# Kernel optimization log

Measured on AMD Instinct MI355X. Metric: run time of the kernel, lower is better.

The kernel has to match this reference:

```python
import jax, jax.numpy as jnp
import numpy as np

B, T, H, D = 1, 2048, 32, 64
SCALE = 0.015625  # 1/64 = 1/head_size
DEG = 2


def setup_inputs() -> dict:
    key = jax.random.key(0)
    k1, k2, k3, k4 = jax.random.split(key, 4)
    q = jax.random.normal(k1, (B, T, H, D), dtype=jnp.float32)
    k = jax.random.normal(k2, (B, T, H, D), dtype=jnp.float32)
    v = jax.random.normal(k3, (B, T, H, D), dtype=jnp.float32)
    # log_G: per-token, per-head log decay (must be <= 0)
    g = -0.1 * jax.random.uniform(k4, (B, T, H), dtype=jnp.float32)
    return {"q": q, "k": k, "v": v, "g": g}


def reference(q, k, v, g):
    # q,k,v: [B,T,H,D]; g: [B,T,H] log-decay (log_G)
    # Power retention, deg=2, attention (quadratic) form for T <= switch_over_seq_len.
    g_cum = jnp.cumsum(g, axis=1)                         # [B,T,H]
    gc = jnp.transpose(g_cum, (0, 2, 1))                  # [B,H,T]
    # decay weight exp(gc[t]-gc[s]) for s<=t, 0 otherwise
    log_decay = gc[:, :, :, None] - gc[:, :, None, :]     # [B,H,T,S]
    causal = jnp.tril(jnp.ones((T, T), dtype=bool))
    decay = jnp.where(causal, jnp.exp(log_decay), 0.0)    # [B,H,T,S]
    qk = jnp.einsum("bthd,bshd->bhts", q, k) * SCALE      # [B,H,T,S]
    w = (qk ** DEG) * decay                               # nonneg scores, deg=2
    num = jnp.einsum("bhts,bshd->bthd", w, v)             # [B,T,H,D]
    denom = jnp.transpose(w.sum(-1), (0, 2, 1))           # [B,T,H]
    out = num / jnp.maximum(denom, 1.0)[..., None]
    return out
```

## Files before the change

kernel.cpp:

```cpp
#include <hip/hip_runtime.h>

#define T_DIM 2048
#define H_DIM 32
#define D_DIM 64
#define SCALE_F 0.015625f
#define TILE_STRIDE 2048

typedef unsigned short ushort;
typedef __attribute__((ext_vector_type(8))) short short8;
typedef __attribute__((ext_vector_type(16))) float f32x16;
typedef __attribute__((ext_vector_type(2))) float f32x2;
typedef __attribute__((ext_vector_type(4))) float f32x4;

#define MFMA32(A, B, C) __builtin_amdgcn_mfma_f32_32x32x16_bf16((A), (B), (C), 0, 0, 0)

__global__ __launch_bounds__(256)
void cumsum_g_kernel(const float* __restrict__ g, float* __restrict__ gc) {
    const int h = blockIdx.x;
    const int tid = threadIdx.x;
    const int PER = T_DIM / 256;

    __shared__ float sums[256];

    float loc[8];
    float run = 0.f;
    const int t0 = tid * PER;
    for (int i = 0; i < PER; ++i) {
        run += g[(size_t)(t0 + i) * H_DIM + h];
        loc[i] = run;
    }
    sums[tid] = run;
    __syncthreads();

    for (int off = 1; off < 256; off <<= 1) {
        float vv = (tid >= off) ? sums[tid - off] : 0.f;
        __syncthreads();
        sums[tid] += vv;
        __syncthreads();
    }
    float excl = (tid == 0) ? 0.f : sums[tid - 1];

    for (int i = 0; i < PER; ++i)
        gc[(size_t)h * T_DIM + t0 + i] = excl + loc[i];
}

__device__ __forceinline__ ushort f2bf(float x) {
    unsigned u = __float_as_uint(x);
    unsigned r = (u + 0x7fffu + ((u >> 16) & 1u)) >> 16;
    return (ushort)r;
}

__global__ __launch_bounds__(256)
void prep_kernel(const float* __restrict__ q, const float* __restrict__ k,
                 const float* __restrict__ v, const float* __restrict__ gc,
                 ushort* __restrict__ qfrag, ushort* __restrict__ kfrag,
                 ushort* __restrict__ vfrag) {
    __shared__ ushort qt_l[64 * 64];
    __shared__ ushort kt_l[64 * 64];

    const int h   = blockIdx.x;
    const int tt  = blockIdx.y;
    const int tid = threadIdx.x;

    {
        const int r    = tid >> 2;
        const int dseg = (tid & 3) * 16;
        const int t    = tt * 64 + r;
        const float gct = gc[(size_t)h * T_DIM + t];
        const float eq = SCALE_F * __expf(0.5f * gct);
        const float ek = __expf(-0.5f * gct);
        const float* qp = q + ((size_t)t * H_DIM + h) * 64 + dseg;
        const float* kp = k + ((size_t)t * H_DIM + h) * 64 + dseg;
        union { ushort u[16]; uint4 uu[2]; } oq, ok;
#pragma unroll
        for (int i = 0; i < 16; ++i) {
            oq.u[i] = f2bf(qp[i] * eq);
            ok.u[i] = f2bf(kp[i] * ek);
        }
        const int c0 = (tid & 3) * 2;
#pragma unroll
        for (int cc = 0; cc < 2; ++cc) {
            const int slot = (c0 + cc) ^ (r & 7);
            *reinterpret_cast<uint4*>(&qt_l[r * 64 + slot * 8]) = oq.uu[cc];
            *reinterpret_cast<uint4*>(&kt_l[r * 64 + slot * 8]) = ok.uu[cc];
        }
    }
    __syncthreads();

#pragma unroll
    for (int n = 0; n < 2; ++n) {
        const int ch   = tid + 256 * n;
        const int l31  = ch & 31;
        const int hi   = (ch >> 5) & 1;
        const int ks   = (ch >> 6) & 3;
        const int t32r = ch >> 8;
        const int row  = t32r * 32 + l31;
        const int slot = (2 * ks + hi) ^ (row & 7);
        uint4 qq = *reinterpret_cast<const uint4*>(&qt_l[row * 64 + slot * 8]);
        uint4 kk = *reinterpret_cast<const uint4*>(&kt_l[row * 64 + slot * 8]);
        const size_t base = ((size_t)h * 64 + tt * 2 + t32r) * TILE_STRIDE
                          + (size_t)(((ks * 2 + hi) * 32) + l31) * 8;
        *reinterpret_cast<uint4*>(qfrag + base) = qq;
        *reinterpret_cast<uint4*>(kfrag + base) = kk;
    }

#pragma unroll
    for (int n = 0; n < 2; ++n) {
        const int c9   = (tid >> 5) + 8 * n;
        const int l31  = tid & 31;
        const int hi   = c9 & 1;
        const int kh2  = (c9 >> 1) & 1;
        const int dblk = (c9 >> 2) & 1;
        const int s32r = c9 >> 3;
        const int tb = tt * 64 + s32r * 32 + kh2 * 16 + hi * 8;
        union { ushort u[8]; uint4 uu; } ov;
#pragma unroll
        for (int j = 0; j < 8; ++j)
            ov.u[j] = f2bf(v[((size_t)(tb + j) * H_DIM + h) * 64 + dblk * 32 + l31]);
        const size_t base = ((size_t)h * 64 + tt * 2 + s32r) * TILE_STRIDE
                          + (size_t)((((dblk * 2 + kh2) * 2 + hi) * 32) + l31) * 8;
        *reinterpret_cast<uint4*>(vfrag + base) = ov.uu;
    }
}

__device__ __forceinline__ short8 ld8(const ushort* p) {
    return *reinterpret_cast<const short8*>(p);
}

__device__ __forceinline__ unsigned cvt_pk_bf16(float lo, float hi) {
    unsigned r;
    asm("v_cvt_pk_bf16_f32 %0, %1, %2" : "=v"(r) : "v"(lo), "v"(hi));
    return r;
}

__device__ __forceinline__ short8 pack_w2(const f32x2* w2) {
    unsigned p0 = cvt_pk_bf16(w2[0][0], w2[0][1]);
    unsigned p1 = cvt_pk_bf16(w2[1][0], w2[1][1]);
    unsigned p2 = cvt_pk_bf16(w2[2][0], w2[2][1]);
    unsigned p3 = cvt_pk_bf16(w2[3][0], w2[3][1]);
    asm("v_permlane32_swap_b32 %0, %1" : "+v"(p0), "+v"(p2));
    asm("v_permlane32_swap_b32 %0, %1" : "+v"(p1), "+v"(p3));
    union { unsigned u[4]; short8 s; } af;
    af.u[0] = p0; af.u[1] = p1; af.u[2] = p2; af.u[3] = p3;
    return af.s;
}

__device__ __forceinline__ void gll16(const void* g, void* l) {
    __builtin_amdgcn_global_load_lds(
        (const __attribute__((address_space(1))) unsigned int*)g,
        (__attribute__((address_space(3))) unsigned int*)l, 16, 0, 0);
}

__device__ __forceinline__ void stage32k(ushort* dst, const char* ksrc,
                                         const char* vsrc, int tid) {
    char* d = (char*)dst + (tid >> 6) * 1024;
    const int lo = tid * 16;
    gll16(ksrc + lo,        d);
    gll16(ksrc + 8192 + lo, d + 8192);
    gll16(vsrc + lo,        d + 16384);
    gll16(vsrc + 8192 + lo, d + 24576);
}

template<int MODE>
__device__ __forceinline__ void unit32(
    const ushort* ldsK, const ushort* ldsV,
    int lofs, int hi, int l31,
    const short8 (&qr)[4], f32x16& o0, f32x16& o1, f32x2& den2)
{
    const short8 kf0 = ld8(ldsK + lofs);
    const short8 kf1 = ld8(ldsK + 512 + lofs);
    const short8 kf2 = ld8(ldsK + 1024 + lofs);
    const short8 kf3 = ld8(ldsK + 1536 + lofs);
    const short8 vf0 = ld8(ldsV + lofs);
    const short8 vf1 = ld8(ldsV + 512 + lofs);
    const short8 vf2 = ld8(ldsV + 1024 + lofs);
    const short8 vf3 = ld8(ldsV + 1536 + lofs);

    f32x16 c;
#pragma unroll
    for (int i = 0; i < 16; ++i) c[i] = 0.f;
    c = MFMA32(kf0, qr[0], c);
    c = MFMA32(kf1, qr[1], c);
    c = MFMA32(kf2, qr[2], c);
    c = MFMA32(kf3, qr[3], c);

    f32x2 w2[8];
#pragma unroll
    for (int i = 0; i < 8; ++i) {
        const int r0 = 2 * i;
        f32x2 x; x[0] = c[r0]; x[1] = c[r0 + 1];
        f32x2 ww = x * x;
        if (MODE == 1) {
            const int sl0 = (r0 & 3) + 8 * (r0 >> 2) + 4 * hi;
            ww[0] = (sl0 <= l31) ? ww[0] : 0.f;
            ww[1] = (sl0 + 1 <= l31) ? ww[1] : 0.f;
        }
        w2[i] = ww;
        den2 += ww;
    }
    const short8 a0 = pack_w2(&w2[0]);
    o0 = MFMA32(a0, vf0, o0);
    o1 = MFMA32(a0, vf2, o1);
    const short8 a1 = pack_w2(&w2[4]);
    o0 = MFMA32(a1, vf1, o0);
    o1 = MFMA32(a1, vf3, o1);
}

__global__ __launch_bounds__(512, 4)
void retention_mfma_kernel(const ushort* __restrict__ qfrag,
                           const ushort* __restrict__ kfrag,
                           const ushort* __restrict__ vfrag,
                           float* __restrict__ out) {
    __shared__ ushort buf[2][16384];

    const int bid = blockIdx.x;
    const int h   = (bid & 7) + 8 * ((bid >> 3) & 3);
    const int r   = bid >> 5;
    const int qb  = (r < 8) ? (2 * r) : (31 - 2 * r + 16 - 16);
    const int qbb = (r < 8) ? (2 * r) : (31 - 2 * (r - 8) - 16 + 16);
    (void)qb; (void)qbb;
    const int QB  = (r < 8) ? (2 * r) : (15 - 2 * (r - 8));

    const int tid = threadIdx.x;
    const int w   = tid >> 6;
    const int qi  = w & 3;
    const int si  = w >> 2;
    const int lane = tid & 63;
    const int hi  = lane >> 5;
    const int l31 = lane & 31;
    const int lofs = hi * 256 + l31 * 8;
    const int myT32 = 4 * QB + qi;

    short8 qr[4];
    {
        const ushort* qp = qfrag + ((size_t)h * 64 + myT32) * TILE_STRIDE;
#pragma unroll
        for (int ks = 0; ks < 4; ++ks) qr[ks] = ld8(qp + ks * 512 + lofs);
    }

    f32x16 o0, o1;
#pragma unroll
    for (int i = 0; i < 16; ++i) { o0[i] = 0.f; o1[i] = 0.f; }
    f32x2 d2; d2[0] = 0.f; d2[1] = 0.f;

    const char* kgb = (const char*)(kfrag + (size_t)h * 64 * TILE_STRIDE);
    const char* vgb = (const char*)(vfrag + (size_t)h * 64 * TILE_STRIDE);

    stage32k(buf[0], kgb, vgb, tid);
    __syncthreads();

    for (int J = 0; J <= QB; ++J) {
        if (J < QB)
            stage32k(buf[(J + 1) & 1], kgb + (size_t)(J + 1) * 16384,
                     vgb + (size_t)(J + 1) * 16384, tid);

        const ushort* bK = buf[J & 1];
        const ushort* bV = bK + 8192;
        const int c1 = 4 * J + si;
        const int c2 = c1 + 2;

        if (c1 < myT32)
            unit32<0>(bK + si * 2048, bV + si * 2048, lofs, hi, l31, qr, o0, o1, d2);
        else if (c1 == myT32)
            unit32<1>(bK + si * 2048, bV + si * 2048, lofs, hi, l31, qr, o0, o1, d2);

        if (c2 < myT32)
            unit32<0>(bK + (2 + si) * 2048, bV + (2 + si) * 2048, lofs, hi, l31, qr, o0, o1, d2);
        else if (c2 == myT32)
            unit32<1>(bK + (2 + si) * 2048, bV + (2 + si) * 2048, lofs, hi, l31, qr, o0, o1, d2);

        __syncthreads();
    }

    float* pm  = (float*)(&buf[0][0]);
    float* pmd = (float*)(&buf[1][0]);

    float den = d2[0] + d2[1];
    den += __shfl_xor(den, 32);
    if (hi == 0) pmd[(qi * 2 + si) * 32 + l31] = den;

    if (si == 0) {
#pragma unroll
        for (int rr = 0; rr < 16; ++rr) {
            const int row = (rr & 3) + 8 * (rr >> 2) + 4 * hi;
            pm[(qi * 32 + row) * 64 + l31]      = o0[rr];
            pm[(qi * 32 + row) * 64 + 32 + l31] = o1[rr];
        }
    }
    __syncthreads();
    if (si == 1) {
#pragma unroll
        for (int rr = 0; rr < 16; ++rr) {
            const int row = (rr & 3) + 8 * (rr >> 2) + 4 * hi;
            pm[(qi * 32 + row) * 64 + l31]      += o0[rr];
            pm[(qi * 32 + row) * 64 + 32 + l31] += o1[rr];
        }
    }
    __syncthreads();

    {
        const int row  = tid >> 2;
        const int qq   = row >> 5;
        const int r32  = row & 31;
        const int dseg = (tid & 3) * 16;
        const float dtot = pmd[(qq * 2 + 0) * 32 + r32] + pmd[(qq * 2 + 1) * 32 + r32];
        const float inv = 1.f / fmaxf(dtot, 1.f);
        const float* src = pm + (qq * 32 + r32) * 64 + dseg;
        float* dst = out + ((size_t)(QB * 128 + row) * H_DIM + h) * 64 + dseg;
#pragma unroll
        for (int jv = 0; jv < 4; ++jv) {
            f32x4 s = *reinterpret_cast<const f32x4*>(src + 4 * jv);
            s *= inv;
            *reinterpret_cast<f32x4*>(dst + 4 * jv) = s;
        }
    }
}

extern "C" void kernel_launch(void* const* d_in, const int* in_sizes, int n_in,
                              void* d_out, int out_size, void* d_ws, size_t ws_size,
                              hipStream_t stream) {
    const float* q = (const float*)d_in[0];
    const float* k = (const float*)d_in[1];
    const float* v = (const float*)d_in[2];
    const float* g = (const float*)d_in[3];
    float* out = (float*)d_out;

    const size_t GC_BYTES = (size_t)H_DIM * T_DIM * sizeof(float);
    const size_t BF_ELEMS = (size_t)H_DIM * T_DIM * D_DIM;

    float* gc = (float*)d_ws;
    ushort* qfrag = (ushort*)((char*)d_ws + GC_BYTES);
    ushort* kfrag = qfrag + BF_ELEMS;
    ushort* vfrag = kfrag + BF_ELEMS;

    cumsum_g_kernel<<<H_DIM, 256, 0, stream>>>(g, gc);
    prep_kernel<<<dim3(H_DIM, T_DIM / 64), 256, 0, stream>>>(q, k, v, gc,
                                                             qfrag, kfrag, vfrag);
    retention_mfma_kernel<<<512, 512, 0, stream>>>(qfrag, kfrag, vfrag, out);
}
```

Baseline: 46.56 us.

## Fuse bf16 prep into retention kernel with register-staged fp32 K/V loads

Removes the separate prep kernel that converted q/k/v to bf16 fragment layout in workspace. The main kernel now loads fp32 Q, K and V directly, applies the decay scaling and converts to bf16 in registers, and writes into a smaller double-buffered LDS tile of 64 keys per step. Global loads for the next tile are issued before compute and written to LDS after it, replacing the async global_load_lds staging. It also reorders block scheduling so the largest query blocks launch first. This saves a launch and a global round trip of the bf16 intermediates. In exchange each block re-reads fp32 K/V (twice the bytes), redoes the conversion, and runs twice as many barrier-synchronised iterations.

```diff
diff --git a/kernel.cpp b/kernel.cpp
--- a/kernel.cpp
+++ b/kernel.cpp
@@ -4,7 +4,7 @@
 #define H_DIM 32
 #define D_DIM 64
 #define SCALE_F 0.015625f
-#define TILE_STRIDE 2048
+#define ROWSTRIDE 2048
 
 typedef unsigned short ushort;
 typedef __attribute__((ext_vector_type(8))) short short8;
@@ -42,85 +42,6 @@
 
     for (int i = 0; i < PER; ++i)
         gc[(size_t)h * T_DIM + t0 + i] = excl + loc[i];
-}
-
-__device__ __forceinline__ ushort f2bf(float x) {
-    unsigned u = __float_as_uint(x);
-    unsigned r = (u + 0x7fffu + ((u >> 16) & 1u)) >> 16;
-    return (ushort)r;
-}
-
-__global__ __launch_bounds__(256)
-void prep_kernel(const float* __restrict__ q, const float* __restrict__ k,
-                 const float* __restrict__ v, const float* __restrict__ gc,
-                 ushort* __restrict__ qfrag, ushort* __restrict__ kfrag,
-                 ushort* __restrict__ vfrag) {
-    __shared__ ushort qt_l[64 * 64];
-    __shared__ ushort kt_l[64 * 64];
-
-    const int h   = blockIdx.x;
-    const int tt  = blockIdx.y;
-    const int tid = threadIdx.x;
-
-    {
-        const int r    = tid >> 2;
-        const int dseg = (tid & 3) * 16;
-        const int t    = tt * 64 + r;
-        const float gct = gc[(size_t)h * T_DIM + t];
-        const float eq = SCALE_F * __expf(0.5f * gct);
-        const float ek = __expf(-0.5f * gct);
-        const float* qp = q + ((size_t)t * H_DIM + h) * 64 + dseg;
-        const float* kp = k + ((size_t)t * H_DIM + h) * 64 + dseg;
-        union { ushort u[16]; uint4 uu[2]; } oq, ok;
-#pragma unroll
-        for (int i = 0; i < 16; ++i) {
-            oq.u[i] = f2bf(qp[i] * eq);
-            ok.u[i] = f2bf(kp[i] * ek);
-        }
-        const int c0 = (tid & 3) * 2;
-#pragma unroll
-        for (int cc = 0; cc < 2; ++cc) {
-            const int slot = (c0 + cc) ^ (r & 7);
-            *reinterpret_cast<uint4*>(&qt_l[r * 64 + slot * 8]) = oq.uu[cc];
-            *reinterpret_cast<uint4*>(&kt_l[r * 64 + slot * 8]) = ok.uu[cc];
-        }
-    }
-    __syncthreads();
-
-#pragma unroll
-    for (int n = 0; n < 2; ++n) {
-        const int ch   = tid + 256 * n;
-        const int l31  = ch & 31;
-        const int hi   = (ch >> 5) & 1;
-        const int ks   = (ch >> 6) & 3;
-        const int t32r = ch >> 8;
-        const int row  = t32r * 32 + l31;
-        const int slot = (2 * ks + hi) ^ (row & 7);
-        uint4 qq = *reinterpret_cast<const uint4*>(&qt_l[row * 64 + slot * 8]);
-        uint4 kk = *reinterpret_cast<const uint4*>(&kt_l[row * 64 + slot * 8]);
-        const size_t base = ((size_t)h * 64 + tt * 2 + t32r) * TILE_STRIDE
-                          + (size_t)(((ks * 2 + hi) * 32) + l31) * 8;
-        *reinterpret_cast<uint4*>(qfrag + base) = qq;
-        *reinterpret_cast<uint4*>(kfrag + base) = kk;
-    }
-
-#pragma unroll
-    for (int n = 0; n < 2; ++n) {
-        const int c9   = (tid >> 5) + 8 * n;
-        const int l31  = tid & 31;
-        const int hi   = c9 & 1;
-        const int kh2  = (c9 >> 1) & 1;
-        const int dblk = (c9 >> 2) & 1;
-        const int s32r = c9 >> 3;
-        const int tb = tt * 64 + s32r * 32 + kh2 * 16 + hi * 8;
-        union { ushort u[8]; uint4 uu; } ov;
-#pragma unroll
-        for (int j = 0; j < 8; ++j)
-            ov.u[j] = f2bf(v[((size_t)(tb + j) * H_DIM + h) * 64 + dblk * 32 + l31]);
-        const size_t base = ((size_t)h * 64 + tt * 2 + s32r) * TILE_STRIDE
-                          + (size_t)((((dblk * 2 + kh2) * 2 + hi) * 32) + l31) * 8;
-        *reinterpret_cast<uint4*>(vfrag + base) = ov.uu;
-    }
 }
 
 __device__ __forceinline__ short8 ld8(const ushort* p) {
@@ -143,22 +64,6 @@
     union { unsigned u[4]; short8 s; } af;
     af.u[0] = p0; af.u[1] = p1; af.u[2] = p2; af.u[3] = p3;
     return af.s;
-}
-
-__device__ __forceinline__ void gll16(const void* g, void* l) {
-    __builtin_amdgcn_global_load_lds(
-        (const __attribute__((address_space(1))) unsigned int*)g,
-        (__attribute__((address_space(3))) unsigned int*)l, 16, 0, 0);
-}
-
-__device__ __forceinline__ void stage32k(ushort* dst, const char* ksrc,
-                                         const char* vsrc, int tid) {
-    char* d = (char*)dst + (tid >> 6) * 1024;
-    const int lo = tid * 16;
-    gll16(ksrc + lo,        d);
-    gll16(ksrc + 8192 + lo, d + 8192);
-    gll16(vsrc + lo,        d + 16384);
-    gll16(vsrc + 8192 + lo, d + 24576);
 }
 
 template<int MODE>
@@ -206,20 +111,68 @@
     o1 = MFMA32(a1, vf3, o1);
 }
 
+struct KStage { f32x4 a, b; float g; };
+struct VStage { float v0, v1, v2, v3, v4, v5, v6, v7; };
+
+__device__ __forceinline__ void issue_k(KStage& s, const float* kg,
+                                        const float* gch, int s0, int tid) {
+    const int r  = tid >> 3;
+    const int d0 = (tid & 7) * 8;
+    const float* p = kg + (size_t)(s0 + r) * ROWSTRIDE + d0;
+    s.a = *reinterpret_cast<const f32x4*>(p);
+    s.b = *reinterpret_cast<const f32x4*>(p + 4);
+    s.g = gch[s0 + r];
+}
+
+__device__ __forceinline__ void write_k(const KStage& s, ushort* bufK, int tid) {
+    const int r  = tid >> 3;
+    const int ks = (tid & 7) >> 1;
+    const int hh = tid & 1;
+    const float ek = __expf(-0.5f * s.g);
+    union { unsigned u[4]; short8 s8; } o;
+    o.u[0] = cvt_pk_bf16(s.a[0] * ek, s.a[1] * ek);
+    o.u[1] = cvt_pk_bf16(s.a[2] * ek, s.a[3] * ek);
+    o.u[2] = cvt_pk_bf16(s.b[0] * ek, s.b[1] * ek);
+    o.u[3] = cvt_pk_bf16(s.b[2] * ek, s.b[3] * ek);
+    *reinterpret_cast<short8*>(bufK + (r >> 5) * 2048 + ks * 512 + hh * 256
+                               + (r & 31) * 8) = o.s8;
+}
+
+__device__ __forceinline__ void issue_v(VStage& s, const float* vg, int s0, int tid) {
+    const int c = tid >> 5, l31 = tid & 31;
+    const int tile = c >> 3, dblk = (c >> 2) & 1, kh2 = (c >> 1) & 1, hiv = c & 1;
+    const int tb = s0 + tile * 32 + kh2 * 16 + hiv * 8;
+    const float* p = vg + (size_t)tb * ROWSTRIDE + dblk * 32 + l31;
+    s.v0 = p[0 * ROWSTRIDE]; s.v1 = p[1 * ROWSTRIDE];
+    s.v2 = p[2 * ROWSTRIDE]; s.v3 = p[3 * ROWSTRIDE];
+    s.v4 = p[4 * ROWSTRIDE]; s.v5 = p[5 * ROWSTRIDE];
+    s.v6 = p[6 * ROWSTRIDE]; s.v7 = p[7 * ROWSTRIDE];
+}
+
+__device__ __forceinline__ void write_v(const VStage& s, ushort* bufV, int tid) {
+    const int c = tid >> 5, l31 = tid & 31;
+    const int tile = c >> 3;
+    const int c3 = c & 7;
+    union { unsigned u[4]; short8 s8; } o;
+    o.u[0] = cvt_pk_bf16(s.v0, s.v1);
+    o.u[1] = cvt_pk_bf16(s.v2, s.v3);
+    o.u[2] = cvt_pk_bf16(s.v4, s.v5);
+    o.u[3] = cvt_pk_bf16(s.v6, s.v7);
+    *reinterpret_cast<short8*>(bufV + tile * 2048 + c3 * 256 + l31 * 8) = o.s8;
+}
+
 __global__ __launch_bounds__(512, 4)
-void retention_mfma_kernel(const ushort* __restrict__ qfrag,
-                           const ushort* __restrict__ kfrag,
-                           const ushort* __restrict__ vfrag,
-                           float* __restrict__ out) {
-    __shared__ ushort buf[2][16384];
+void retention_fused_kernel(const float* __restrict__ q,
+                            const float* __restrict__ k,
+                            const float* __restrict__ v,
+                            const float* __restrict__ gc,
+                            float* __restrict__ out) {
+    __shared__ ushort buf[2][8192];
+    __shared__ float pmd[8 * 32];
 
     const int bid = blockIdx.x;
-    const int h   = (bid & 7) + 8 * ((bid >> 3) & 3);
-    const int r   = bid >> 5;
-    const int qb  = (r < 8) ? (2 * r) : (31 - 2 * r + 16 - 16);
-    const int qbb = (r < 8) ? (2 * r) : (31 - 2 * (r - 8) - 16 + 16);
-    (void)qb; (void)qbb;
-    const int QB  = (r < 8) ? (2 * r) : (15 - 2 * (r - 8));
+    const int h   = bid & 31;
+    const int QB  = 15 - (bid >> 5);
 
     const int tid = threadIdx.x;
     const int w   = tid >> 6;
@@ -231,11 +184,26 @@
     const int lofs = hi * 256 + l31 * 8;
     const int myT32 = 4 * QB + qi;
 
+    const float* gch = gc + (size_t)h * T_DIM;
+    const float* kg  = k + h * 64;
+    const float* vg  = v + h * 64;
+
     short8 qr[4];
     {
-        const ushort* qp = qfrag + ((size_t)h * 64 + myT32) * TILE_STRIDE;
-#pragma unroll
-        for (int ks = 0; ks < 4; ++ks) qr[ks] = ld8(qp + ks * 512 + lofs);
+        const int t = myT32 * 32 + l31;
+        const float eq = SCALE_F * __expf(0.5f * gch[t]);
+        const float* qrow = q + (size_t)t * ROWSTRIDE + h * 64 + hi * 8;
+#pragma unroll
+        for (int ks = 0; ks < 4; ++ks) {
+            f32x4 fa = *reinterpret_cast<const f32x4*>(qrow + ks * 16);
+            f32x4 fb = *reinterpret_cast<const f32x4*>(qrow + ks * 16 + 4);
+            union { unsigned u[4]; short8 s8; } o;
+            o.u[0] = cvt_pk_bf16(fa[0] * eq, fa[1] * eq);
+            o.u[1] = cvt_pk_bf16(fa[2] * eq, fa[3] * eq);
+            o.u[2] = cvt_pk_bf16(fb[0] * eq, fb[1] * eq);
+            o.u[3] = cvt_pk_bf16(fb[2] * eq, fb[3] * eq);
+            qr[ks] = o.s8;
+        }
     }
 
     f32x16 o0, o1;
@@ -243,37 +211,38 @@
     for (int i = 0; i < 16; ++i) { o0[i] = 0.f; o1[i] = 0.f; }
     f32x2 d2; d2[0] = 0.f; d2[1] = 0.f;
 
-    const char* kgb = (const char*)(kfrag + (size_t)h * 64 * TILE_STRIDE);
-    const char* vgb = (const char*)(vfrag + (size_t)h * 64 * TILE_STRIDE);
-
-    stage32k(buf[0], kgb, vgb, tid);
+    const int NJ = 2 * QB + 2;
+
+    KStage kst; VStage vst;
+    issue_k(kst, kg, gch, 0, tid);
+    issue_v(vst, vg, 0, tid);
+    write_k(kst, buf[0], tid);
+    write_v(vst, buf[0] + 4096, tid);
     __syncthreads();
 
-    for (int J = 0; J <= QB; ++J) {
-        if (J < QB)
-            stage32k(buf[(J + 1) & 1], kgb + (size_t)(J + 1) * 16384,
-                     vgb + (size_t)(J + 1) * 16384, tid);
-
-        const ushort* bK = buf[J & 1];
-        const ushort* bV = bK + 8192;
-        const int c1 = 4 * J + si;
-        const int c2 = c1 + 2;
+    for (int J = 0; J < NJ; ++J) {
+        const int cur = J & 1;
+        if (J + 1 < NJ) {
+            issue_k(kst, kg, gch, (J + 1) * 64, tid);
+            issue_v(vst, vg, (J + 1) * 64, tid);
+        }
+        const ushort* bK = buf[cur];
+        const ushort* bV = buf[cur] + 4096;
+        const int c1 = 2 * J + si;
 
         if (c1 < myT32)
             unit32<0>(bK + si * 2048, bV + si * 2048, lofs, hi, l31, qr, o0, o1, d2);
         else if (c1 == myT32)
             unit32<1>(bK + si * 2048, bV + si * 2048, lofs, hi, l31, qr, o0, o1, d2);
 
-        if (c2 < myT32)
-            unit32<0>(bK + (2 + si) * 2048, bV + (2 + si) * 2048, lofs, hi, l31, qr, o0, o1, d2);
-        else if (c2 == myT32)
-            unit32<1>(bK + (2 + si) * 2048, bV + (2 + si) * 2048, lofs, hi, l31, qr, o0, o1, d2);
-
+        if (J + 1 < NJ) {
+            write_k(kst, buf[cur ^ 1], tid);
+            write_v(vst, buf[cur ^ 1] + 4096, tid);
+        }
         __syncthreads();
     }
 
-    float* pm  = (float*)(&buf[0][0]);
-    float* pmd = (float*)(&buf[1][0]);
+    float* pm = (float*)&buf[0][0];
 
     float den = d2[0] + d2[1];
     den += __shfl_xor(den, 32);
@@ -303,7 +272,8 @@
         const int qq   = row >> 5;
         const int r32  = row & 31;
         const int dseg = (tid & 3) * 16;
-        const float dtot = pmd[(qq * 2 + 0) * 32 + r32] + pmd[(qq * 2 + 1) * 32 + r32];
+        const float dtot = pmd[(qq * 2 + 0) * 32 + r32]
+                         + pmd[(qq * 2 + 1) * 32 + r32];
         const float inv = 1.f / fmaxf(dtot, 1.f);
         const float* src = pm + (qq * 32 + r32) * 64 + dseg;
         float* dst = out + ((size_t)(QB * 128 + row) * H_DIM + h) * 64 + dseg;
@@ -325,16 +295,8 @@
     const float* g = (const float*)d_in[3];
     float* out = (float*)d_out;
 
-    const size_t GC_BYTES = (size_t)H_DIM * T_DIM * sizeof(float);
-    const size_t BF_ELEMS = (size_t)H_DIM * T_DIM * D_DIM;
-
     float* gc = (float*)d_ws;
-    ushort* qfrag = (ushort*)((char*)d_ws + GC_BYTES);
-    ushort* kfrag = qfrag + BF_ELEMS;
-    ushort* vfrag = kfrag + BF_ELEMS;
 
     cumsum_g_kernel<<<H_DIM, 256, 0, stream>>>(g, gc);
-    prep_kernel<<<dim3(H_DIM, T_DIM / 64), 256, 0, stream>>>(q, k, v, gc,
-                                                             qfrag, kfrag, vfrag);
-    retention_mfma_kernel<<<512, 512, 0, stream>>>(qfrag, kfrag, vfrag, out);
-}
+    retention_fused_kernel<<<512, 512, 0, stream>>>(q, k, v, gc, out);
+}
```

After: 50.05 us. 1.07x slower.

## Load K/V fragments directly from global memory and rebalance query tiles per block

Applied to the files above, without the earlier changes.

The main kernel no longer stages K/V tiles into LDS with a double buffer and barriers. Each wave now reads its K/V fragments straight from global memory (relying on L2 reuse) for a single 32-row query tile. Each 256-thread block pairs a long tile (63-pair) with a short one (pair) so the causal work per block is even, and the two waves on a tile split the key tiles by parity. The epilogue is simplified to a single LDS reduction that writes the output from registers. This removes LDS staging and the per-iteration syncs, at the cost of more global/L2 traffic and less data sharing across waves.

```diff
diff --git a/kernel.cpp b/kernel.cpp
--- a/kernel.cpp
+++ b/kernel.cpp
@@ -145,36 +145,20 @@
     return af.s;
 }
 
-__device__ __forceinline__ void gll16(const void* g, void* l) {
-    __builtin_amdgcn_global_load_lds(
-        (const __attribute__((address_space(1))) unsigned int*)g,
-        (__attribute__((address_space(3))) unsigned int*)l, 16, 0, 0);
-}
-
-__device__ __forceinline__ void stage32k(ushort* dst, const char* ksrc,
-                                         const char* vsrc, int tid) {
-    char* d = (char*)dst + (tid >> 6) * 1024;
-    const int lo = tid * 16;
-    gll16(ksrc + lo,        d);
-    gll16(ksrc + 8192 + lo, d + 8192);
-    gll16(vsrc + lo,        d + 16384);
-    gll16(vsrc + 8192 + lo, d + 24576);
-}
-
 template<int MODE>
-__device__ __forceinline__ void unit32(
-    const ushort* ldsK, const ushort* ldsV,
+__device__ __forceinline__ void unitD(
+    const ushort* __restrict__ kb, const ushort* __restrict__ vb,
     int lofs, int hi, int l31,
     const short8 (&qr)[4], f32x16& o0, f32x16& o1, f32x2& den2)
 {
-    const short8 kf0 = ld8(ldsK + lofs);
-    const short8 kf1 = ld8(ldsK + 512 + lofs);
-    const short8 kf2 = ld8(ldsK + 1024 + lofs);
-    const short8 kf3 = ld8(ldsK + 1536 + lofs);
-    const short8 vf0 = ld8(ldsV + lofs);
-    const short8 vf1 = ld8(ldsV + 512 + lofs);
-    const short8 vf2 = ld8(ldsV + 1024 + lofs);
-    const short8 vf3 = ld8(ldsV + 1536 + lofs);
+    const short8 kf0 = ld8(kb + lofs);
+    const short8 kf1 = ld8(kb + 512 + lofs);
+    const short8 kf2 = ld8(kb + 1024 + lofs);
+    const short8 kf3 = ld8(kb + 1536 + lofs);
+    const short8 vf0 = ld8(vb + lofs);
+    const short8 vf1 = ld8(vb + 512 + lofs);
+    const short8 vf2 = ld8(vb + 1024 + lofs);
+    const short8 vf3 = ld8(vb + 1536 + lofs);
 
     f32x16 c;
 #pragma unroll
@@ -206,36 +190,32 @@
     o1 = MFMA32(a1, vf3, o1);
 }
 
-__global__ __launch_bounds__(512, 4)
-void retention_mfma_kernel(const ushort* __restrict__ qfrag,
+__global__ __launch_bounds__(256, 4)
+void retention_main_kernel(const ushort* __restrict__ qfrag,
                            const ushort* __restrict__ kfrag,
                            const ushort* __restrict__ vfrag,
                            float* __restrict__ out) {
-    __shared__ ushort buf[2][16384];
-
-    const int bid = blockIdx.x;
-    const int h   = (bid & 7) + 8 * ((bid >> 3) & 3);
-    const int r   = bid >> 5;
-    const int qb  = (r < 8) ? (2 * r) : (31 - 2 * r + 16 - 16);
-    const int qbb = (r < 8) ? (2 * r) : (31 - 2 * (r - 8) - 16 + 16);
-    (void)qb; (void)qbb;
-    const int QB  = (r < 8) ? (2 * r) : (15 - 2 * (r - 8));
-
-    const int tid = threadIdx.x;
-    const int w   = tid >> 6;
-    const int qi  = w & 3;
-    const int si  = w >> 2;
+    __shared__ float lds_o[2][32][64];
+    __shared__ float lds_d[2][32];
+
+    const int bid  = blockIdx.x;
+    const int h    = bid & 31;
+    const int pair = bid >> 5;
+    const int tid  = threadIdx.x;
+    const int w    = tid >> 6;
     const int lane = tid & 63;
-    const int hi  = lane >> 5;
-    const int l31 = lane & 31;
+    const int hi   = lane >> 5;
+    const int l31  = lane & 31;
     const int lofs = hi * 256 + l31 * 8;
-    const int myT32 = 4 * QB + qi;
+
+    const int m   = (w < 2) ? (63 - pair) : pair;
+    const int par = w & 1;
 
     short8 qr[4];
     {
-        const ushort* qp = qfrag + ((size_t)h * 64 + myT32) * TILE_STRIDE;
-#pragma unroll
-        for (int ks = 0; ks < 4; ++ks) qr[ks] = ld8(qp + ks * 512 + lofs);
+        const ushort* qb = qfrag + ((size_t)h * 64 + m) * TILE_STRIDE;
+#pragma unroll
+        for (int ks = 0; ks < 4; ++ks) qr[ks] = ld8(qb + ks * 512 + lofs);
     }
 
     f32x16 o0, o1;
@@ -243,75 +223,44 @@
     for (int i = 0; i < 16; ++i) { o0[i] = 0.f; o1[i] = 0.f; }
     f32x2 d2; d2[0] = 0.f; d2[1] = 0.f;
 
-    const char* kgb = (const char*)(kfrag + (size_t)h * 64 * TILE_STRIDE);
-    const char* vgb = (const char*)(vfrag + (size_t)h * 64 * TILE_STRIDE);
-
-    stage32k(buf[0], kgb, vgb, tid);
-    __syncthreads();
-
-    for (int J = 0; J <= QB; ++J) {
-        if (J < QB)
-            stage32k(buf[(J + 1) & 1], kgb + (size_t)(J + 1) * 16384,
-                     vgb + (size_t)(J + 1) * 16384, tid);
-
-        const ushort* bK = buf[J & 1];
-        const ushort* bV = bK + 8192;
-        const int c1 = 4 * J + si;
-        const int c2 = c1 + 2;
-
-        if (c1 < myT32)
-            unit32<0>(bK + si * 2048, bV + si * 2048, lofs, hi, l31, qr, o0, o1, d2);
-        else if (c1 == myT32)
-            unit32<1>(bK + si * 2048, bV + si * 2048, lofs, hi, l31, qr, o0, o1, d2);
-
-        if (c2 < myT32)
-            unit32<0>(bK + (2 + si) * 2048, bV + (2 + si) * 2048, lofs, hi, l31, qr, o0, o1, d2);
-        else if (c2 == myT32)
-            unit32<1>(bK + (2 + si) * 2048, bV + (2 + si) * 2048, lofs, hi, l31, qr, o0, o1, d2);
-
-        __syncthreads();
-    }
-
-    float* pm  = (float*)(&buf[0][0]);
-    float* pmd = (float*)(&buf[1][0]);
+    const ushort* khb = kfrag + (size_t)h * 64 * TILE_STRIDE;
+    const ushort* vhb = vfrag + (size_t)h * 64 * TILE_STRIDE;
+
+    int st = par;
+    for (; st < m; st += 2)
+        unitD<0>(khb + (size_t)st * TILE_STRIDE, vhb + (size_t)st * TILE_STRIDE,
+                 lofs, hi, l31, qr, o0, o1, d2);
+    if (st == m)
+        unitD<1>(khb + (size_t)m * TILE_STRIDE, vhb + (size_t)m * TILE_STRIDE,
+                 lofs, hi, l31, qr, o0, o1, d2);
 
     float den = d2[0] + d2[1];
     den += __shfl_xor(den, 32);
-    if (hi == 0) pmd[(qi * 2 + si) * 32 + l31] = den;
-
-    if (si == 0) {
+
+    const int slot = w >> 1;
+    if (par == 1) {
 #pragma unroll
         for (int rr = 0; rr < 16; ++rr) {
             const int row = (rr & 3) + 8 * (rr >> 2) + 4 * hi;
-            pm[(qi * 32 + row) * 64 + l31]      = o0[rr];
-            pm[(qi * 32 + row) * 64 + 32 + l31] = o1[rr];
-        }
+            lds_o[slot][row][l31]      = o0[rr];
+            lds_o[slot][row][32 + l31] = o1[rr];
+        }
+        if (hi == 0) lds_d[slot][l31] = den;
     }
     __syncthreads();
-    if (si == 1) {
+    if (par == 0) {
+        const float dtot = den + lds_d[slot][l31];
 #pragma unroll
         for (int rr = 0; rr < 16; ++rr) {
             const int row = (rr & 3) + 8 * (rr >> 2) + 4 * hi;
-            pm[(qi * 32 + row) * 64 + l31]      += o0[rr];
-            pm[(qi * 32 + row) * 64 + 32 + l31] += o1[rr];
-        }
-    }
-    __syncthreads();
-
-    {
-        const int row  = tid >> 2;
-        const int qq   = row >> 5;
-        const int r32  = row & 31;
-        const int dseg = (tid & 3) * 16;
-        const float dtot = pmd[(qq * 2 + 0) * 32 + r32] + pmd[(qq * 2 + 1) * 32 + r32];
-        const float inv = 1.f / fmaxf(dtot, 1.f);
-        const float* src = pm + (qq * 32 + r32) * 64 + dseg;
-        float* dst = out + ((size_t)(QB * 128 + row) * H_DIM + h) * 64 + dseg;
-#pragma unroll
-        for (int jv = 0; jv < 4; ++jv) {
-            f32x4 s = *reinterpret_cast<const f32x4*>(src + 4 * jv);
-            s *= inv;
-            *reinterpret_cast<f32x4*>(dst + 4 * jv) = s;
+            const float s0 = o0[rr] + lds_o[slot][row][l31];
+            const float s1 = o1[rr] + lds_o[slot][row][32 + l31];
+            const float dt = __shfl(dtot, row);
+            const float inv = 1.f / fmaxf(dt, 1.f);
+            const int t = m * 32 + row;
+            float* op = out + ((size_t)t * H_DIM + h) * 64;
+            op[l31]      = s0 * inv;
+            op[32 + l31] = s1 * inv;
         }
     }
 }
@@ -336,5 +285,5 @@
     cumsum_g_kernel<<<H_DIM, 256, 0, stream>>>(g, gc);
     prep_kernel<<<dim3(H_DIM, T_DIM / 64), 256, 0, stream>>>(q, k, v, gc,
                                                              qfrag, kfrag, vfrag);
-    retention_mfma_kernel<<<512, 512, 0, stream>>>(qfrag, kfrag, vfrag, out);
-}
+    retention_main_kernel<<<1024, 256, 0, stream>>>(qfrag, kfrag, vfrag, out);
+}
```

Result: slower. 52.48 us (+12.7%).
